# Kernel optimization log

Hardware: AMD Instinct MI355X
Metric: run time of the kernel (lower is better)

The kernel has to match this reference:

```python
import jax, jax.numpy as jnp
import numpy as np

B, S, D_IN = 4, 2048, 1024
EMBED, H = 1024, 16
HD = EMBED // H  # 64


def setup_inputs() -> dict:
    key = jax.random.key(0)
    k1, k2, k3 = jax.random.split(key, 3)
    x = jax.random.normal(k1, (B, S, D_IN), dtype=jnp.float32)
    # xavier_uniform for torch Linear weight [out, in]
    lim_qkv = float(np.sqrt(6.0 / (D_IN + 3 * EMBED)))
    W_qkv = jax.random.uniform(k2, (3 * EMBED, D_IN), minval=-lim_qkv, maxval=lim_qkv, dtype=jnp.float32)
    b_qkv = jnp.zeros((3 * EMBED,), dtype=jnp.float32)
    lim_o = float(np.sqrt(6.0 / (EMBED + EMBED)))
    W_out = jax.random.uniform(k3, (EMBED, EMBED), minval=-lim_o, maxval=lim_o, dtype=jnp.float32)
    b_out = jnp.zeros((EMBED,), dtype=jnp.float32)
    return {"x": x, "W_qkv": W_qkv, "b_qkv": b_qkv, "W_out": W_out, "b_out": b_out}


def reference(x, W_qkv, b_qkv, W_out, b_out):
    b, s, _ = x.shape
    qkv = x @ W_qkv.T + b_qkv                      # [b, s, 3*embed]
    # einops 'b s (h c d) -> c b h s d': fused dim groups as (h, 3, d)
    qkv = qkv.reshape(b, s, H, 3, HD)
    qkv = jnp.transpose(qkv, (3, 0, 2, 1, 4))      # [3, b, h, s, d]
    q, k, v = qkv[0], qkv[1], qkv[2]
    scale = 1.0 / jnp.sqrt(jnp.asarray(HD, dtype=q.dtype))
    logits = jnp.einsum('bhqd,bhkd->bhqk', q, k) * scale
    attn = jax.nn.softmax(logits, axis=-1)
    vals = jnp.einsum('bhqk,bhkd->bhqd', attn, v)  # [b, h, s, d]
    vals = jnp.transpose(vals, (0, 2, 1, 3)).reshape(b, s, EMBED)
    return vals @ W_out.T + b_out
```

## Files before the change

### kernel.cpp

```cpp
#include <hip/hip_runtime.h>
#include <hip/hip_bf16.h>
#include <stdint.h>

#define B_   4
#define S_   2048
#define DIN  1024
#define EMB  1024
#define H_   16
#define HD_  64
#define TOK  (B_*S_)
#define NQKV 3072

using bf16  = __hip_bfloat16;
using f32x4 = __attribute__((ext_vector_type(4))) float;
using f32x16 = __attribute__((ext_vector_type(16))) float;
using s16x8 = __attribute__((ext_vector_type(8))) short;
using bf16x8 = __attribute__((ext_vector_type(8))) __bf16;

__device__ __forceinline__ f32x4 mfma16(s16x8 a, s16x8 b, f32x4 c) {
  return __builtin_amdgcn_mfma_f32_16x16x32_bf16(
      __builtin_bit_cast(bf16x8, a), __builtin_bit_cast(bf16x8, b), c, 0, 0, 0);
}
__device__ __forceinline__ f32x16 mfma32(s16x8 a, s16x8 b, f32x16 c) {
  return __builtin_amdgcn_mfma_f32_32x32x16_bf16(
      __builtin_bit_cast(bf16x8, a), __builtin_bit_cast(bf16x8, b), c, 0, 0, 0);
}

__device__ __forceinline__ void gload_lds16(const void* g, void* l) {
  __builtin_amdgcn_global_load_lds(
      (const __attribute__((address_space(1))) uint32_t*)g,
      (__attribute__((address_space(3))) uint32_t*)l, 16, 0, 0);
}

__device__ __forceinline__ uint32_t cvtpk_bf16(float lo, float hi) {
  uint32_t r;
  asm("v_cvt_pk_bf16_f32 %0, %1, %2" : "=v"(r) : "v"(lo), "v"(hi));
  return r;
}
__device__ __forceinline__ void plswap32(uint32_t &a, uint32_t &b) {
  asm("v_permlane32_swap_b32 %0, %1" : "+v"(a), "+v"(b));
}

union U8 { s16x8 v; bf16 b[8]; };
union PaU { uint32_t w[4]; s16x8 v; };

__global__ __launch_bounds__(256) void cvt_all(const float* __restrict__ x,
                                               const float* __restrict__ wqkv,
                                               const float* __restrict__ wout,
                                               bf16* __restrict__ xb,
                                               bf16* __restrict__ wqkvb,
                                               bf16* __restrict__ woutb) {
  int b = blockIdx.x;
  const float* in; bf16* out; int base;
  if (b < 4096)      { in = x;    out = xb;    base = b; }
  else if (b < 5632) { in = wqkv; out = wqkvb; base = b - 4096; }
  else               { in = wout; out = woutb; base = b - 5632; }
  int i = (base * 256 + (int)threadIdx.x) * 8;
  float4 a = *(const float4*)(in + i);
  float4 c = *(const float4*)(in + i + 4);
  U8 u;
  u.b[0] = __float2bfloat16(a.x); u.b[1] = __float2bfloat16(a.y);
  u.b[2] = __float2bfloat16(a.z); u.b[3] = __float2bfloat16(a.w);
  u.b[4] = __float2bfloat16(c.x); u.b[5] = __float2bfloat16(c.y);
  u.b[6] = __float2bfloat16(c.z); u.b[7] = __float2bfloat16(c.w);
  *(s16x8*)(out + i) = u.v;
}

template<int MODE>
__global__ __launch_bounds__(256) void gemm_bt(
    const bf16* __restrict__ A, const bf16* __restrict__ Bw,
    const float* __restrict__ bias,
    bf16* __restrict__ outQK, bf16* __restrict__ outV,
    float* __restrict__ outF, int N, int K)
{
  const int tid  = threadIdx.x;
  const int lane = tid & 63;
  const int w    = tid >> 6;
  const int wm   = w >> 1, wn = w & 1;
  const int bn0  = blockIdx.x * 128;
  const int bm0  = blockIdx.y * 128;

  __shared__ __align__(16) bf16 As[128 * 64];
  __shared__ __align__(16) bf16 Bs[128 * 64];

  f32x4 acc[4][4];
  const f32x4 zero = {0.f, 0.f, 0.f, 0.f};
  for (int mt = 0; mt < 4; ++mt)
    for (int nt = 0; nt < 4; ++nt) acc[mt][nt] = zero;

  for (int kt = 0; kt < K; kt += 64) {
    for (int i = 0; i < 4; ++i) {
      int c   = i * 256 + tid;
      int row = c >> 3, p = c & 7;
      int sc  = p ^ (row & 7);
      gload_lds16(A + (size_t)(bm0 + row) * K + kt + sc * 8, (char*)As + c * 16);
      gload_lds16(Bw + (size_t)(bn0 + row) * K + kt + sc * 8, (char*)Bs + c * 16);
    }
    __syncthreads();

    s16x8 af[4][2], bfr[4][2];
    for (int mt = 0; mt < 4; ++mt)
      for (int kk = 0; kk < 2; ++kk) {
        int row  = wm * 64 + mt * 16 + (lane & 15);
        int byte = row * 128 + (((kk * 4 + (lane >> 4)) ^ (row & 7)) << 4);
        af[mt][kk] = *(const s16x8*)((const char*)As + byte);
      }
    for (int nt = 0; nt < 4; ++nt)
      for (int kk = 0; kk < 2; ++kk) {
        int row  = wn * 64 + nt * 16 + (lane & 15);
        int byte = row * 128 + (((kk * 4 + (lane >> 4)) ^ (row & 7)) << 4);
        bfr[nt][kk] = *(const s16x8*)((const char*)Bs + byte);
      }
    for (int kk = 0; kk < 2; ++kk)
      for (int mt = 0; mt < 4; ++mt)
        for (int nt = 0; nt < 4; ++nt)
          acc[mt][nt] = mfma16(af[mt][kk], bfr[nt][kk], acc[mt][nt]);
    __syncthreads();
  }

  const int col_l = lane & 15;
  const int rgrp  = lane >> 4;
  for (int mt = 0; mt < 4; ++mt)
    for (int nt = 0; nt < 4; ++nt) {
      int n0  = bn0 + wn * 64 + nt * 16;
      int col = n0 + col_l;
      float bv = bias[col];
      if (MODE == 0) {
        int h = col / 192, rem = col % 192;
        int cc = rem / 64, d = rem % 64;
        for (int r = 0; r < 4; ++r) {
          int row = bm0 + wm * 64 + mt * 16 + rgrp * 4 + r;
          bf16 bvv = __float2bfloat16(acc[mt][nt][r] + bv);
          if (cc == 2) {
            int bb = row >> 11, s = row & 2047;
            outV[(((size_t)bb * H_ + h) * HD_ + d) * S_ + s] = bvv;
          } else {
            outQK[(size_t)row * NQKV + col] = bvv;
          }
        }
      } else {
        for (int r = 0; r < 4; ++r) {
          int row = bm0 + wm * 64 + mt * 16 + rgrp * 4 + r;
          outF[(size_t)row * EMB + col] = acc[mt][nt][r] + bv;
        }
      }
    }
}

__global__ __launch_bounds__(512, 2) void attn2(const bf16* __restrict__ qkvb,
                                                const bf16* __restrict__ vb,
                                                bf16* __restrict__ ob)
{
  const int tid = threadIdx.x, lane = tid & 63, w = tid >> 6;
  const int hi = lane >> 5, l31 = lane & 31;
  const int f  = blockIdx.x;
  const int bh = (f & 7) | (((f >> 6) & 7) << 3);
  const int qt = (f >> 3) & 7;
  const int bb = bh >> 4, h = bh & 15;
  const int q0 = qt * 256;
  const size_t tokbase = (size_t)bb * S_;

  __shared__ __align__(16) char KsB[2][8 * 1040];
  __shared__ __align__(16) char VtsB[2][8 * 1040];

  s16x8 qf[4];
  {
    const int qrow = q0 + w * 32 + l31;
    const bf16* qp = qkvb + (tokbase + qrow) * NQKV + h * 192 + hi * 8;
    #pragma unroll
    for (int ks = 0; ks < 4; ++ks) {
      U8 u; u.v = *(const s16x8*)(qp + ks * 16);
      #pragma unroll
      for (int j = 0; j < 8; ++j)
        u.b[j] = __float2bfloat16(__bfloat162float(u.b[j]) * 0.18033688011112042f);
      qf[ks] = u.v;
    }
  }

  f32x16 zero16;
  #pragma unroll
  for (int i = 0; i < 16; ++i) zero16[i] = 0.f;
  f32x16 oA = zero16, oB = zero16;
  f32x16 nm16 = zero16;
  float l0 = 0.f;

  const bf16* Kbase = qkvb + tokbase * NQKV + h * 192 + 64;
  const bf16* Vbase = vb + (size_t)bh * HD_ * S_;

  const int srow = tid >> 3, sp = tid & 7;
  const bf16* kSrc = Kbase + (size_t)srow * NQKV + sp * 8;
  const bf16* vSrc = Vbase + (size_t)srow * S_ + sp * 8;
  const int   sByte = sp * 1040 + srow * 16;

  s16x8 kreg, vreg;
  auto LOAD = [&](int t) {
    kreg = *(const s16x8*)(kSrc + (size_t)t * 64 * NQKV);
    vreg = *(const s16x8*)(vSrc + (size_t)t * 64);
  };
  auto WRITE = [&](int b) {
    *(s16x8*)(KsB[b] + sByte) = kreg;
    *(s16x8*)(VtsB[b] + sByte) = vreg;
  };

  LOAD(0);
  WRITE(0);
  __syncthreads();

  int cur = 0;
  for (int t = 0; t < S_ / 64; ++t) {
    if (t < S_ / 64 - 1) LOAD(t + 1);

    f32x16 pA, pB;
    #pragma unroll
    for (int ks = 0; ks < 4; ++ks) {
      const char* kb = KsB[cur] + (2 * ks + hi) * 1040;
      {
        s16x8 kf = *(const s16x8*)(kb + l31 * 16);
        pA = mfma32(kf, qf[ks], ks == 0 ? nm16 : pA);
      }
      {
        s16x8 kf = *(const s16x8*)(kb + 512 + l31 * 16);
        pB = mfma32(kf, qf[ks], ks == 0 ? nm16 : pB);
      }
    }

    float mx8[8];
    #pragma unroll
    for (int i = 0; i < 8; ++i)
      mx8[i] = fmaxf(fmaxf(pA[i], pA[i + 8]), fmaxf(pB[i], pB[i + 8]));
    float pmax = fmaxf(fmaxf(fmaxf(mx8[0], mx8[4]), fmaxf(mx8[1], mx8[5])),
                       fmaxf(fmaxf(mx8[2], mx8[6]), fmaxf(mx8[3], mx8[7])));
    pmax = fmaxf(pmax, __shfl_xor(pmax, 32));

    if (__any(pmax > 11.0f)) {
      float al = __builtin_amdgcn_exp2f(-pmax);
      l0 *= al;
      #pragma unroll
      for (int r = 0; r < 16; ++r) {
        float alr = __shfl(al, (r & 3) + 8 * (r >> 2) + 4 * hi);
        oA[r] *= alr; oB[r] *= alr;
      }
      #pragma unroll
      for (int r = 0; r < 16; ++r) { pA[r] -= pmax; pB[r] -= pmax; }
      #pragma unroll
      for (int i = 0; i < 16; ++i) nm16[i] -= pmax;
    }

    #pragma unroll
    for (int r = 0; r < 16; ++r) {
      pA[r] = __builtin_amdgcn_exp2f(pA[r]);
      pB[r] = __builtin_amdgcn_exp2f(pB[r]);
    }
    float s8[8];
    #pragma unroll
    for (int i = 0; i < 8; ++i)
      s8[i] = (pA[i] + pA[i + 8]) + (pB[i] + pB[i + 8]);
    l0 += ((s8[0] + s8[1]) + (s8[2] + s8[3])) +
          ((s8[4] + s8[5]) + (s8[6] + s8[7]));

    #pragma unroll
    for (int s = 0; s < 4; ++s) {
      const int sub = s & 1;
      const f32x16 &ph = (s < 2) ? pA : pB;
      uint32_t L0 = cvtpk_bf16(ph[8 * sub + 0], ph[8 * sub + 1]);
      uint32_t L1 = cvtpk_bf16(ph[8 * sub + 2], ph[8 * sub + 3]);
      uint32_t H0 = cvtpk_bf16(ph[8 * sub + 4], ph[8 * sub + 5]);
      uint32_t H1 = cvtpk_bf16(ph[8 * sub + 6], ph[8 * sub + 7]);
      plswap32(L0, H0);
      plswap32(L1, H1);
      PaU pa; pa.w[0] = L0; pa.w[1] = L1; pa.w[2] = H0; pa.w[3] = H1;
      const char* vbp = VtsB[cur] + (2 * s + hi) * 1040;
      {
        s16x8 vf = *(const s16x8*)(vbp + l31 * 16);
        oA = mfma32(pa.v, vf, oA);
      }
      {
        s16x8 vf = *(const s16x8*)(vbp + 512 + l31 * 16);
        oB = mfma32(pa.v, vf, oB);
      }
    }

    if (t < S_ / 64 - 1) WRITE(cur ^ 1);
    __syncthreads();
    cur ^= 1;
  }

  float l0t = l0 + __shfl_xor(l0, 32);
  float inv = 1.0f / l0t;
  #pragma unroll
  for (int r = 0; r < 16; ++r) {
    int q = (r & 3) + 8 * (r >> 2) + 4 * hi;
    float invr = __shfl(inv, q);
    int qrow = q0 + w * 32 + q;
    bf16* op = ob + (tokbase + qrow) * EMB + h * 64 + l31;
    op[0]  = __float2bfloat16(oA[r] * invr);
    op[32] = __float2bfloat16(oB[r] * invr);
  }
}

extern "C" void kernel_launch(void* const* d_in, const int* in_sizes, int n_in,
                              void* d_out, int out_size, void* d_ws, size_t ws_size,
                              hipStream_t stream) {
  const float* x    = (const float*)d_in[0];
  const float* Wqkv = (const float*)d_in[1];
  const float* bqkv = (const float*)d_in[2];
  const float* Wout = (const float*)d_in[3];
  const float* bout = (const float*)d_in[4];
  float* out = (float*)d_out;

  char* ws = (char*)d_ws;
  bf16* xb    = (bf16*)(ws);
  bf16* wqkvb = (bf16*)(ws + 16777216);
  bf16* woutb = (bf16*)(ws + 23068672);
  bf16* qkvb  = (bf16*)(ws + 25165824);
  bf16* vb    = (bf16*)(ws + 75497472);
  bf16* ob    = xb;

  cvt_all<<<dim3(6144), 256, 0, stream>>>(x, Wqkv, Wout, xb, wqkvb, woutb);

  gemm_bt<0><<<dim3(NQKV / 128, TOK / 128), 256, 0, stream>>>(
      xb, wqkvb, bqkv, qkvb, vb, nullptr, NQKV, DIN);

  attn2<<<dim3(512), 512, 0, stream>>>(qkvb, vb, ob);

  gemm_bt<1><<<dim3(EMB / 128, TOK / 128), 256, 0, stream>>>(
      ob, woutb, bout, nullptr, nullptr, out, EMB, EMB);
}
```

Measured before the change: 204.3 us.

## Process two 32-row query tiles per wave in attention to reuse K/V fragments

Each wave now handles 64 query rows as two 32-row sub-tiles, and the block covers 512 queries instead of 256. The grid shrinks to 256 blocks and launch bounds drop to one block per SIMD group. Each K and V fragment read from shared memory now feeds twice as many MFMAs, which halves LDS reads and global K/V tile traffic per query. In exchange, register pressure roughly doubles. Only 256 blocks of 512 threads may underfill the 256 CUs, with fewer waves per CU to hide latency.

```diff
diff --git a/kernel.cpp b/kernel.cpp
--- a/kernel.cpp
+++ b/kernel.cpp
@@ -147,25 +147,25 @@
     }
 }
 
-__global__ __launch_bounds__(512, 2) void attn2(const bf16* __restrict__ qkvb,
+__global__ __launch_bounds__(512, 1) void attn2(const bf16* __restrict__ qkvb,
                                                 const bf16* __restrict__ vb,
                                                 bf16* __restrict__ ob)
 {
   const int tid = threadIdx.x, lane = tid & 63, w = tid >> 6;
   const int hi = lane >> 5, l31 = lane & 31;
   const int f  = blockIdx.x;
-  const int bh = (f & 7) | (((f >> 6) & 7) << 3);
-  const int qt = (f >> 3) & 7;
+  const int bh = (f & 7) | ((f >> 5) << 3);
+  const int qt = (f >> 3) & 3;
   const int bb = bh >> 4, h = bh & 15;
-  const int q0 = qt * 256;
+  const int q0 = qt * 512;
   const size_t tokbase = (size_t)bb * S_;
 
   __shared__ __align__(16) char KsB[2][8 * 1040];
   __shared__ __align__(16) char VtsB[2][8 * 1040];
 
-  s16x8 qf[4];
+  s16x8 qf0[4], qf1[4];
   {
-    const int qrow = q0 + w * 32 + l31;
+    const int qrow = q0 + w * 64 + l31;
     const bf16* qp = qkvb + (tokbase + qrow) * NQKV + h * 192 + hi * 8;
     #pragma unroll
     for (int ks = 0; ks < 4; ++ks) {
@@ -173,16 +173,25 @@
       #pragma unroll
       for (int j = 0; j < 8; ++j)
         u.b[j] = __float2bfloat16(__bfloat162float(u.b[j]) * 0.18033688011112042f);
-      qf[ks] = u.v;
+      qf0[ks] = u.v;
+    }
+    const bf16* qp1 = qp + (size_t)32 * NQKV;
+    #pragma unroll
+    for (int ks = 0; ks < 4; ++ks) {
+      U8 u; u.v = *(const s16x8*)(qp1 + ks * 16);
+      #pragma unroll
+      for (int j = 0; j < 8; ++j)
+        u.b[j] = __float2bfloat16(__bfloat162float(u.b[j]) * 0.18033688011112042f);
+      qf1[ks] = u.v;
     }
   }
 
   f32x16 zero16;
   #pragma unroll
   for (int i = 0; i < 16; ++i) zero16[i] = 0.f;
-  f32x16 oA = zero16, oB = zero16;
-  f32x16 nm16 = zero16;
-  float l0 = 0.f;
+  f32x16 oA0 = zero16, oB0 = zero16, oA1 = zero16, oB1 = zero16;
+  f32x16 nm0 = zero16, nm1 = zero16;
+  float l00 = 0.f, l01 = 0.f;
 
   const bf16* Kbase = qkvb + tokbase * NQKV + h * 192 + 64;
   const bf16* Vbase = vb + (size_t)bh * HD_ * S_;
@@ -210,74 +219,104 @@
   for (int t = 0; t < S_ / 64; ++t) {
     if (t < S_ / 64 - 1) LOAD(t + 1);
 
-    f32x16 pA, pB;
+    f32x16 pA0, pB0, pA1, pB1;
     #pragma unroll
     for (int ks = 0; ks < 4; ++ks) {
       const char* kb = KsB[cur] + (2 * ks + hi) * 1040;
-      {
-        s16x8 kf = *(const s16x8*)(kb + l31 * 16);
-        pA = mfma32(kf, qf[ks], ks == 0 ? nm16 : pA);
-      }
-      {
-        s16x8 kf = *(const s16x8*)(kb + 512 + l31 * 16);
-        pB = mfma32(kf, qf[ks], ks == 0 ? nm16 : pB);
-      }
-    }
-
-    float mx8[8];
-    #pragma unroll
-    for (int i = 0; i < 8; ++i)
-      mx8[i] = fmaxf(fmaxf(pA[i], pA[i + 8]), fmaxf(pB[i], pB[i + 8]));
-    float pmax = fmaxf(fmaxf(fmaxf(mx8[0], mx8[4]), fmaxf(mx8[1], mx8[5])),
-                       fmaxf(fmaxf(mx8[2], mx8[6]), fmaxf(mx8[3], mx8[7])));
-    pmax = fmaxf(pmax, __shfl_xor(pmax, 32));
-
-    if (__any(pmax > 11.0f)) {
-      float al = __builtin_amdgcn_exp2f(-pmax);
-      l0 *= al;
+      s16x8 klo = *(const s16x8*)(kb + l31 * 16);
+      s16x8 khi = *(const s16x8*)(kb + 512 + l31 * 16);
+      pA0 = mfma32(klo, qf0[ks], ks == 0 ? nm0 : pA0);
+      pB0 = mfma32(khi, qf0[ks], ks == 0 ? nm0 : pB0);
+      pA1 = mfma32(klo, qf1[ks], ks == 0 ? nm1 : pA1);
+      pB1 = mfma32(khi, qf1[ks], ks == 0 ? nm1 : pB1);
+    }
+
+    float mx0[8], mx1[8];
+    #pragma unroll
+    for (int i = 0; i < 8; ++i) {
+      mx0[i] = fmaxf(fmaxf(pA0[i], pA0[i + 8]), fmaxf(pB0[i], pB0[i + 8]));
+      mx1[i] = fmaxf(fmaxf(pA1[i], pA1[i + 8]), fmaxf(pB1[i], pB1[i + 8]));
+    }
+    float pmax0 = fmaxf(fmaxf(fmaxf(mx0[0], mx0[4]), fmaxf(mx0[1], mx0[5])),
+                        fmaxf(fmaxf(mx0[2], mx0[6]), fmaxf(mx0[3], mx0[7])));
+    float pmax1 = fmaxf(fmaxf(fmaxf(mx1[0], mx1[4]), fmaxf(mx1[1], mx1[5])),
+                        fmaxf(fmaxf(mx1[2], mx1[6]), fmaxf(mx1[3], mx1[7])));
+    pmax0 = fmaxf(pmax0, __shfl_xor(pmax0, 32));
+    pmax1 = fmaxf(pmax1, __shfl_xor(pmax1, 32));
+
+    if (__any(fmaxf(pmax0, pmax1) > 11.0f)) {
+      float al0 = __builtin_amdgcn_exp2f(-pmax0);
+      float al1 = __builtin_amdgcn_exp2f(-pmax1);
+      l00 *= al0; l01 *= al1;
       #pragma unroll
       for (int r = 0; r < 16; ++r) {
-        float alr = __shfl(al, (r & 3) + 8 * (r >> 2) + 4 * hi);
-        oA[r] *= alr; oB[r] *= alr;
-      }
-      #pragma unroll
-      for (int r = 0; r < 16; ++r) { pA[r] -= pmax; pB[r] -= pmax; }
-      #pragma unroll
-      for (int i = 0; i < 16; ++i) nm16[i] -= pmax;
+        int crow = (r & 3) + 8 * (r >> 2) + 4 * hi;
+        float a0 = __shfl(al0, crow), a1 = __shfl(al1, crow);
+        oA0[r] *= a0; oB0[r] *= a0;
+        oA1[r] *= a1; oB1[r] *= a1;
+      }
+      #pragma unroll
+      for (int r = 0; r < 16; ++r) {
+        pA0[r] -= pmax0; pB0[r] -= pmax0;
+        pA1[r] -= pmax1; pB1[r] -= pmax1;
+      }
+      #pragma unroll
+      for (int i = 0; i < 16; ++i) { nm0[i] -= pmax0; nm1[i] -= pmax1; }
     }
 
     #pragma unroll
     for (int r = 0; r < 16; ++r) {
-      pA[r] = __builtin_amdgcn_exp2f(pA[r]);
-      pB[r] = __builtin_amdgcn_exp2f(pB[r]);
-    }
-    float s8[8];
-    #pragma unroll
-    for (int i = 0; i < 8; ++i)
-      s8[i] = (pA[i] + pA[i + 8]) + (pB[i] + pB[i + 8]);
-    l0 += ((s8[0] + s8[1]) + (s8[2] + s8[3])) +
-          ((s8[4] + s8[5]) + (s8[6] + s8[7]));
-
+      pA0[r] = __builtin_amdgcn_exp2f(pA0[r]);
+      pB0[r] = __builtin_amdgcn_exp2f(pB0[r]);
+      pA1[r] = __builtin_amdgcn_exp2f(pA1[r]);
+      pB1[r] = __builtin_amdgcn_exp2f(pB1[r]);
+    }
+    {
+      float s80[8], s81[8];
+      #pragma unroll
+      for (int i = 0; i < 8; ++i) {
+        s80[i] = (pA0[i] + pA0[i + 8]) + (pB0[i] + pB0[i + 8]);
+        s81[i] = (pA1[i] + pA1[i + 8]) + (pB1[i] + pB1[i + 8]);
+      }
+      l00 += ((s80[0] + s80[1]) + (s80[2] + s80[3])) +
+             ((s80[4] + s80[5]) + (s80[6] + s80[7]));
+      l01 += ((s81[0] + s81[1]) + (s81[2] + s81[3])) +
+             ((s81[4] + s81[5]) + (s81[6] + s81[7]));
+    }
+
+    PaU pa0[4], pa1[4];
     #pragma unroll
     for (int s = 0; s < 4; ++s) {
       const int sub = s & 1;
-      const f32x16 &ph = (s < 2) ? pA : pB;
-      uint32_t L0 = cvtpk_bf16(ph[8 * sub + 0], ph[8 * sub + 1]);
-      uint32_t L1 = cvtpk_bf16(ph[8 * sub + 2], ph[8 * sub + 3]);
-      uint32_t H0 = cvtpk_bf16(ph[8 * sub + 4], ph[8 * sub + 5]);
-      uint32_t H1 = cvtpk_bf16(ph[8 * sub + 6], ph[8 * sub + 7]);
-      plswap32(L0, H0);
-      plswap32(L1, H1);
-      PaU pa; pa.w[0] = L0; pa.w[1] = L1; pa.w[2] = H0; pa.w[3] = H1;
+      {
+        const f32x16 &ph = (s < 2) ? pA0 : pB0;
+        uint32_t L0 = cvtpk_bf16(ph[8 * sub + 0], ph[8 * sub + 1]);
+        uint32_t L1 = cvtpk_bf16(ph[8 * sub + 2], ph[8 * sub + 3]);
+        uint32_t H0 = cvtpk_bf16(ph[8 * sub + 4], ph[8 * sub + 5]);
+        uint32_t H1 = cvtpk_bf16(ph[8 * sub + 6], ph[8 * sub + 7]);
+        plswap32(L0, H0); plswap32(L1, H1);
+        pa0[s].w[0] = L0; pa0[s].w[1] = L1; pa0[s].w[2] = H0; pa0[s].w[3] = H1;
+      }
+      {
+        const f32x16 &ph = (s < 2) ? pA1 : pB1;
+        uint32_t L0 = cvtpk_bf16(ph[8 * sub + 0], ph[8 * sub + 1]);
+        uint32_t L1 = cvtpk_bf16(ph[8 * sub + 2], ph[8 * sub + 3]);
+        uint32_t H0 = cvtpk_bf16(ph[8 * sub + 4], ph[8 * sub + 5]);
+        uint32_t H1 = cvtpk_bf16(ph[8 * sub + 6], ph[8 * sub + 7]);
+        plswap32(L0, H0); plswap32(L1, H1);
+        pa1[s].w[0] = L0; pa1[s].w[1] = L1; pa1[s].w[2] = H0; pa1[s].w[3] = H1;
+      }
+    }
+
+    #pragma unroll
+    for (int s = 0; s < 4; ++s) {
       const char* vbp = VtsB[cur] + (2 * s + hi) * 1040;
-      {
-        s16x8 vf = *(const s16x8*)(vbp + l31 * 16);
-        oA = mfma32(pa.v, vf, oA);
-      }
-      {
-        s16x8 vf = *(const s16x8*)(vbp + 512 + l31 * 16);
-        oB = mfma32(pa.v, vf, oB);
-      }
+      s16x8 vlo = *(const s16x8*)(vbp + l31 * 16);
+      s16x8 vhi = *(const s16x8*)(vbp + 512 + l31 * 16);
+      oA0 = mfma32(pa0[s].v, vlo, oA0);
+      oB0 = mfma32(pa0[s].v, vhi, oB0);
+      oA1 = mfma32(pa1[s].v, vlo, oA1);
+      oB1 = mfma32(pa1[s].v, vhi, oB1);
     }
 
     if (t < S_ / 64 - 1) WRITE(cur ^ 1);
@@ -285,16 +324,20 @@
     cur ^= 1;
   }
 
-  float l0t = l0 + __shfl_xor(l0, 32);
-  float inv = 1.0f / l0t;
+  float l0t0 = l00 + __shfl_xor(l00, 32);
+  float l0t1 = l01 + __shfl_xor(l01, 32);
+  float inv0 = 1.0f / l0t0, inv1 = 1.0f / l0t1;
   #pragma unroll
   for (int r = 0; r < 16; ++r) {
     int q = (r & 3) + 8 * (r >> 2) + 4 * hi;
-    float invr = __shfl(inv, q);
-    int qrow = q0 + w * 32 + q;
-    bf16* op = ob + (tokbase + qrow) * EMB + h * 64 + l31;
-    op[0]  = __float2bfloat16(oA[r] * invr);
-    op[32] = __float2bfloat16(oB[r] * invr);
+    float ir0 = __shfl(inv0, q), ir1 = __shfl(inv1, q);
+    int qrow = q0 + w * 64 + q;
+    bf16* op0 = ob + (tokbase + qrow) * EMB + h * 64 + l31;
+    op0[0]  = __float2bfloat16(oA0[r] * ir0);
+    op0[32] = __float2bfloat16(oB0[r] * ir0);
+    bf16* op1 = op0 + (size_t)32 * EMB;
+    op1[0]  = __float2bfloat16(oA1[r] * ir1);
+    op1[32] = __float2bfloat16(oB1[r] * ir1);
   }
 }
 
@@ -321,7 +364,7 @@
   gemm_bt<0><<<dim3(NQKV / 128, TOK / 128), 256, 0, stream>>>(
       xb, wqkvb, bqkv, qkvb, vb, nullptr, NQKV, DIN);
 
-  attn2<<<dim3(512), 512, 0, stream>>>(qkvb, vb, ob);
+  attn2<<<dim3(256), 512, 0, stream>>>(qkvb, vb, ob);
 
   gemm_bt<1><<<dim3(EMB / 128, TOK / 128), 256, 0, stream>>>(
       ob, woutb, bout, nullptr, nullptr, out, EMB, EMB);
```

New measurement: 195.9 us. 1.04x faster.
